# Performance work log

Measured on AMD Instinct MI355X. Metric: run time of the kernel, lower is better.

The kernel has to match this reference:

```python
import jax, jax.numpy as jnp
import numpy as np

GAMMA = 1.0

def setup_inputs() -> dict:
    key = jax.random.key(0)
    kx, ky = jax.random.split(key)
    x = jax.random.normal(kx, (8192, 64), dtype=jnp.float32)
    y = jax.random.normal(ky, (8192, 64), dtype=jnp.float32)
    return {"x": x, "y": y}

def reference(x, y):
    # RBF kernel K[b,a] = exp(-gamma * ||x_b - y_a||^2)
    # broadcast intermediate of the naive formulation (same math).
    x_sq = jnp.sum(x * x, axis=-1)                    # (B,)
    y_sq = jnp.sum(y * y, axis=-1)                    # (A,)
    xy = jnp.einsum('bd,ad->ba', x, y)                # (B, A) GEMM
    dist_sq = x_sq[:, None] + y_sq[None, :] - 2.0 * xy
    dist_sq = jnp.maximum(dist_sq, 0.0)               # numeric floor
    return jnp.exp(-GAMMA * dist_sq)
```

## Files before the change

### kernel.cpp

```cpp
#include <hip/hip_runtime.h>

#define D    64
#define BM   128
#define BN   128
#define NROW 8192

typedef _Float16 f16x8 __attribute__((ext_vector_type(8)));
typedef float    f32x4 __attribute__((ext_vector_type(4)));

__global__ __launch_bounds__(256) void rbf_rowsq(const float* __restrict__ x,
                                                 const float* __restrict__ y,
                                                 float* __restrict__ sq) {
    int tid = blockIdx.x * blockDim.x + threadIdx.x;
    const float* src = (tid < NROW) ? x : y;
    int row = tid & (NROW - 1);
    const float4* p = reinterpret_cast<const float4*>(src + row * D);
    float s = 0.f;
#pragma unroll
    for (int i = 0; i < D / 4; ++i) {
        float4 v = p[i];
        s = fmaf(v.x, v.x, s);
        s = fmaf(v.y, v.y, s);
        s = fmaf(v.z, v.z, s);
        s = fmaf(v.w, v.w, s);
    }
    sq[tid] = s;
}

__global__ __launch_bounds__(256, 2) void rbf_main(const float* __restrict__ x,
                                                   const float* __restrict__ y,
                                                   const float* __restrict__ sq,
                                                   float* __restrict__ out) {
    __shared__ __align__(16) char smem[65536];
    char* const XH = smem;
    char* const XL = smem + 16384;
    char* const YH = smem + 32768;
    char* const YL = smem + 49152;

    const int t    = threadIdx.x;
    const int row0 = blockIdx.y * BM;
    const int col0 = blockIdx.x * BN;

    {
        const int r    = t & 127;
        const int half = t >> 7;
        const int swz  = (r & 7) << 4;
        const int rowoff = r * 128;
        const float* xp = x + (size_t)(row0 + r) * D + half * 32;
        const float* yp = y + (size_t)(col0 + r) * D + half * 32;
#pragma unroll
        for (int it = 0; it < 4; ++it) {
            const int off = rowoff + ((half * 64 + it * 16) ^ swz);
            float4 a0 = *reinterpret_cast<const float4*>(xp + it * 8);
            float4 a1 = *reinterpret_cast<const float4*>(xp + it * 8 + 4);
            float4 b0 = *reinterpret_cast<const float4*>(yp + it * 8);
            float4 b1 = *reinterpret_cast<const float4*>(yp + it * 8 + 4);
            float xa[8] = {a0.x, a0.y, a0.z, a0.w, a1.x, a1.y, a1.z, a1.w};
            float yb[8] = {b0.x, b0.y, b0.z, b0.w, b1.x, b1.y, b1.z, b1.w};
            f16x8 xh, xl, yh, yl;
#pragma unroll
            for (int j = 0; j < 8; ++j) {
                _Float16 h = (_Float16)xa[j];
                xh[j] = h;
                xl[j] = (_Float16)(xa[j] - (float)h);
                _Float16 g = (_Float16)yb[j];
                yh[j] = g;
                yl[j] = (_Float16)(yb[j] - (float)g);
            }
            *reinterpret_cast<f16x8*>(XH + off) = xh;
            *reinterpret_cast<f16x8*>(XL + off) = xl;
            *reinterpret_cast<f16x8*>(YH + off) = yh;
            *reinterpret_cast<f16x8*>(YL + off) = yl;
        }
    }
    __syncthreads();

    const int lane = t & 63;
    const int w    = t >> 6;
    const int l15  = lane & 15;
    const int lg   = lane >> 4;
    const int swz  = (l15 & 7) << 4;

    const int arow0 = w * 32 + l15;
    const int arow1 = arow0 + 16;

    f32x4 acc[2][8];
#pragma unroll
    for (int i = 0; i < 2; ++i)
#pragma unroll
        for (int j = 0; j < 8; ++j) acc[i][j] = (f32x4){0.f, 0.f, 0.f, 0.f};

#pragma unroll
    for (int kh = 0; kh < 2; ++kh) {
        const int dsw = (kh * 64 + lg * 16) ^ swz;
        f16x8 ah0 = *reinterpret_cast<const f16x8*>(XH + arow0 * 128 + dsw);
        f16x8 ah1 = *reinterpret_cast<const f16x8*>(XH + arow1 * 128 + dsw);
        f16x8 al0 = *reinterpret_cast<const f16x8*>(XL + arow0 * 128 + dsw);
        f16x8 al1 = *reinterpret_cast<const f16x8*>(XL + arow1 * 128 + dsw);
#pragma unroll
        for (int nt = 0; nt < 8; ++nt) {
            const int boff = (nt * 16 + l15) * 128 + dsw;
            f16x8 bh = *reinterpret_cast<const f16x8*>(YH + boff);
            f16x8 bl = *reinterpret_cast<const f16x8*>(YL + boff);
            acc[0][nt] = __builtin_amdgcn_mfma_f32_16x16x32_f16(ah0, bh, acc[0][nt], 0, 0, 0);
            acc[1][nt] = __builtin_amdgcn_mfma_f32_16x16x32_f16(ah1, bh, acc[1][nt], 0, 0, 0);
            acc[0][nt] = __builtin_amdgcn_mfma_f32_16x16x32_f16(ah0, bl, acc[0][nt], 0, 0, 0);
            acc[1][nt] = __builtin_amdgcn_mfma_f32_16x16x32_f16(ah1, bl, acc[1][nt], 0, 0, 0);
            acc[0][nt] = __builtin_amdgcn_mfma_f32_16x16x32_f16(al0, bh, acc[0][nt], 0, 0, 0);
            acc[1][nt] = __builtin_amdgcn_mfma_f32_16x16x32_f16(al1, bh, acc[1][nt], 0, 0, 0);
        }
    }

    float xsqv[2][4], ysqv[8];
#pragma unroll
    for (int mt = 0; mt < 2; ++mt)
#pragma unroll
        for (int r = 0; r < 4; ++r)
            xsqv[mt][r] = sq[row0 + w * 32 + mt * 16 + lg * 4 + r];
#pragma unroll
    for (int nt = 0; nt < 8; ++nt)
        ysqv[nt] = sq[NROW + col0 + nt * 16 + l15];

#pragma unroll
    for (int mt = 0; mt < 2; ++mt) {
#pragma unroll
        for (int r = 0; r < 4; ++r) {
            const int rowg = row0 + w * 32 + mt * 16 + lg * 4 + r;
            float* op = out + (size_t)rowg * NROW + col0 + l15;
#pragma unroll
            for (int nt = 0; nt < 8; ++nt) {
                float d2 = fmaf(-2.f, acc[mt][nt][r], xsqv[mt][r] + ysqv[nt]);
                d2 = fmaxf(d2, 0.f);
                op[nt * 16] = __expf(-d2);
            }
        }
    }
}

extern "C" void kernel_launch(void* const* d_in, const int* in_sizes, int n_in,
                              void* d_out, int out_size, void* d_ws, size_t ws_size,
                              hipStream_t stream) {
    const float* x = (const float*)d_in[0];
    const float* y = (const float*)d_in[1];
    float* out = (float*)d_out;
    float* sq  = (float*)d_ws;

    rbf_rowsq<<<64, 256, 0, stream>>>(x, y, sq);
    rbf_main<<<dim3(NROW / BN, NROW / BM), 256, 0, stream>>>(x, y, sq, out);
}
```

Baseline: 72.69 us.

## Fuse row-norm kernel into main RBF kernel, keep X in registers, vectorize stores

Removes the separate row-squared-norm kernel and computes x and y norms inside the main kernel, with x norms reduced by lane shuffles and y norms kept in shared memory. X fragments are now loaded straight into registers, so shared memory drops to 32KB and occupancy can rise to 3 blocks per CU. The MFMA operands are swapped so each lane holds 4 consecutive output columns, which allows float4 output stores in place of scalar ones. The cost is redundant norm computation in every block and higher register pressure.

```diff
diff --git a/kernel.cpp b/kernel.cpp
--- a/kernel.cpp
+++ b/kernel.cpp
@@ -1,138 +1,121 @@
 #include <hip/hip_runtime.h>
 
 #define D    64
-#define BM   128
-#define BN   128
 #define NROW 8192
 
 typedef _Float16 f16x8 __attribute__((ext_vector_type(8)));
 typedef float    f32x4 __attribute__((ext_vector_type(4)));
 
-__global__ __launch_bounds__(256) void rbf_rowsq(const float* __restrict__ x,
-                                                 const float* __restrict__ y,
-                                                 float* __restrict__ sq) {
-    int tid = blockIdx.x * blockDim.x + threadIdx.x;
-    const float* src = (tid < NROW) ? x : y;
-    int row = tid & (NROW - 1);
-    const float4* p = reinterpret_cast<const float4*>(src + row * D);
-    float s = 0.f;
-#pragma unroll
-    for (int i = 0; i < D / 4; ++i) {
-        float4 v = p[i];
-        s = fmaf(v.x, v.x, s);
-        s = fmaf(v.y, v.y, s);
-        s = fmaf(v.z, v.z, s);
-        s = fmaf(v.w, v.w, s);
-    }
-    sq[tid] = s;
-}
-
-__global__ __launch_bounds__(256, 2) void rbf_main(const float* __restrict__ x,
-                                                   const float* __restrict__ y,
-                                                   const float* __restrict__ sq,
-                                                   float* __restrict__ out) {
-    __shared__ __align__(16) char smem[65536];
-    char* const XH = smem;
-    char* const XL = smem + 16384;
-    char* const YH = smem + 32768;
-    char* const YL = smem + 49152;
+__global__ __launch_bounds__(256, 3) void rbf_fused(const float* __restrict__ x,
+                                                    const float* __restrict__ y,
+                                                    float* __restrict__ out) {
+    __shared__ __align__(16) char YH[16384];
+    __shared__ __align__(16) char YL[16384];
+    __shared__ float Ysq0[128];
+    __shared__ float Ysq1[128];
 
     const int t    = threadIdx.x;
-    const int row0 = blockIdx.y * BM;
-    const int col0 = blockIdx.x * BN;
+    const int col0 = blockIdx.x * 128;
+    const int row0 = blockIdx.y * 128;
 
     {
         const int r    = t & 127;
         const int half = t >> 7;
         const int swz  = (r & 7) << 4;
-        const int rowoff = r * 128;
-        const float* xp = x + (size_t)(row0 + r) * D + half * 32;
         const float* yp = y + (size_t)(col0 + r) * D + half * 32;
+        float ssq = 0.f;
 #pragma unroll
         for (int it = 0; it < 4; ++it) {
-            const int off = rowoff + ((half * 64 + it * 16) ^ swz);
-            float4 a0 = *reinterpret_cast<const float4*>(xp + it * 8);
-            float4 a1 = *reinterpret_cast<const float4*>(xp + it * 8 + 4);
             float4 b0 = *reinterpret_cast<const float4*>(yp + it * 8);
             float4 b1 = *reinterpret_cast<const float4*>(yp + it * 8 + 4);
-            float xa[8] = {a0.x, a0.y, a0.z, a0.w, a1.x, a1.y, a1.z, a1.w};
-            float yb[8] = {b0.x, b0.y, b0.z, b0.w, b1.x, b1.y, b1.z, b1.w};
-            f16x8 xh, xl, yh, yl;
+            float v[8] = {b0.x, b0.y, b0.z, b0.w, b1.x, b1.y, b1.z, b1.w};
+            f16x8 h, l;
 #pragma unroll
             for (int j = 0; j < 8; ++j) {
-                _Float16 h = (_Float16)xa[j];
-                xh[j] = h;
-                xl[j] = (_Float16)(xa[j] - (float)h);
-                _Float16 g = (_Float16)yb[j];
-                yh[j] = g;
-                yl[j] = (_Float16)(yb[j] - (float)g);
+                _Float16 hh = (_Float16)v[j];
+                h[j] = hh;
+                l[j] = (_Float16)(v[j] - (float)hh);
+                ssq  = fmaf(v[j], v[j], ssq);
             }
-            *reinterpret_cast<f16x8*>(XH + off) = xh;
-            *reinterpret_cast<f16x8*>(XL + off) = xl;
-            *reinterpret_cast<f16x8*>(YH + off) = yh;
-            *reinterpret_cast<f16x8*>(YL + off) = yl;
+            const int off = r * 128 + ((half * 64 + it * 16) ^ swz);
+            *reinterpret_cast<f16x8*>(YH + off) = h;
+            *reinterpret_cast<f16x8*>(YL + off) = l;
         }
+        if (half == 0) Ysq0[r] = ssq; else Ysq1[r] = ssq;
     }
-    __syncthreads();
 
     const int lane = t & 63;
     const int w    = t >> 6;
     const int l15  = lane & 15;
     const int lg   = lane >> 4;
-    const int swz  = (l15 & 7) << 4;
 
-    const int arow0 = w * 32 + l15;
-    const int arow1 = arow0 + 16;
+    f16x8 xh[2][2], xl[2][2];
+    float xsq[2];
+#pragma unroll
+    for (int i = 0; i < 2; ++i) {
+        const float* xp = x + (size_t)(row0 + w * 32 + i * 16 + l15) * D + lg * 8;
+        float s = 0.f;
+#pragma unroll
+        for (int kh = 0; kh < 2; ++kh) {
+            float4 a0 = *reinterpret_cast<const float4*>(xp + kh * 32);
+            float4 a1 = *reinterpret_cast<const float4*>(xp + kh * 32 + 4);
+            float v[8] = {a0.x, a0.y, a0.z, a0.w, a1.x, a1.y, a1.z, a1.w};
+#pragma unroll
+            for (int j = 0; j < 8; ++j) {
+                _Float16 hh = (_Float16)v[j];
+                xh[i][kh][j] = hh;
+                xl[i][kh][j] = (_Float16)(v[j] - (float)hh);
+                s = fmaf(v[j], v[j], s);
+            }
+        }
+        s += __shfl_xor(s, 16);
+        s += __shfl_xor(s, 32);
+        xsq[i] = s;
+    }
+    __syncthreads();
 
     f32x4 acc[2][8];
 #pragma unroll
     for (int i = 0; i < 2; ++i)
 #pragma unroll
-        for (int j = 0; j < 8; ++j) acc[i][j] = (f32x4){0.f, 0.f, 0.f, 0.f};
+        for (int nt = 0; nt < 8; ++nt) acc[i][nt] = (f32x4){0.f, 0.f, 0.f, 0.f};
 
+    const int swzA = (l15 & 7) << 4;
 #pragma unroll
     for (int kh = 0; kh < 2; ++kh) {
-        const int dsw = (kh * 64 + lg * 16) ^ swz;
-        f16x8 ah0 = *reinterpret_cast<const f16x8*>(XH + arow0 * 128 + dsw);
-        f16x8 ah1 = *reinterpret_cast<const f16x8*>(XH + arow1 * 128 + dsw);
-        f16x8 al0 = *reinterpret_cast<const f16x8*>(XL + arow0 * 128 + dsw);
-        f16x8 al1 = *reinterpret_cast<const f16x8*>(XL + arow1 * 128 + dsw);
+        const int dsw = (kh * 64 + lg * 16) ^ swzA;
 #pragma unroll
         for (int nt = 0; nt < 8; ++nt) {
-            const int boff = (nt * 16 + l15) * 128 + dsw;
-            f16x8 bh = *reinterpret_cast<const f16x8*>(YH + boff);
-            f16x8 bl = *reinterpret_cast<const f16x8*>(YL + boff);
-            acc[0][nt] = __builtin_amdgcn_mfma_f32_16x16x32_f16(ah0, bh, acc[0][nt], 0, 0, 0);
-            acc[1][nt] = __builtin_amdgcn_mfma_f32_16x16x32_f16(ah1, bh, acc[1][nt], 0, 0, 0);
-            acc[0][nt] = __builtin_amdgcn_mfma_f32_16x16x32_f16(ah0, bl, acc[0][nt], 0, 0, 0);
-            acc[1][nt] = __builtin_amdgcn_mfma_f32_16x16x32_f16(ah1, bl, acc[1][nt], 0, 0, 0);
-            acc[0][nt] = __builtin_amdgcn_mfma_f32_16x16x32_f16(al0, bh, acc[0][nt], 0, 0, 0);
-            acc[1][nt] = __builtin_amdgcn_mfma_f32_16x16x32_f16(al1, bh, acc[1][nt], 0, 0, 0);
+            const int aoff = (nt * 16 + l15) * 128 + dsw;
+            f16x8 yh = *reinterpret_cast<const f16x8*>(YH + aoff);
+            f16x8 yl = *reinterpret_cast<const f16x8*>(YL + aoff);
+            acc[0][nt] = __builtin_amdgcn_mfma_f32_16x16x32_f16(yh, xh[0][kh], acc[0][nt], 0, 0, 0);
+            acc[1][nt] = __builtin_amdgcn_mfma_f32_16x16x32_f16(yh, xh[1][kh], acc[1][nt], 0, 0, 0);
+            acc[0][nt] = __builtin_amdgcn_mfma_f32_16x16x32_f16(yl, xh[0][kh], acc[0][nt], 0, 0, 0);
+            acc[1][nt] = __builtin_amdgcn_mfma_f32_16x16x32_f16(yl, xh[1][kh], acc[1][nt], 0, 0, 0);
+            acc[0][nt] = __builtin_amdgcn_mfma_f32_16x16x32_f16(yh, xl[0][kh], acc[0][nt], 0, 0, 0);
+            acc[1][nt] = __builtin_amdgcn_mfma_f32_16x16x32_f16(yh, xl[1][kh], acc[1][nt], 0, 0, 0);
         }
     }
 
-    float xsqv[2][4], ysqv[8];
 #pragma unroll
-    for (int mt = 0; mt < 2; ++mt)
+    for (int nt = 0; nt < 8; ++nt) {
+        const int c = nt * 16 + lg * 4;
+        float4 p0 = *reinterpret_cast<const float4*>(&Ysq0[c]);
+        float4 p1 = *reinterpret_cast<const float4*>(&Ysq1[c]);
+        float ysqv[4] = {p0.x + p1.x, p0.y + p1.y, p0.z + p1.z, p0.w + p1.w};
 #pragma unroll
-        for (int r = 0; r < 4; ++r)
-            xsqv[mt][r] = sq[row0 + w * 32 + mt * 16 + lg * 4 + r];
+        for (int i = 0; i < 2; ++i) {
+            const int rowg = row0 + w * 32 + i * 16 + l15;
+            float e[4];
 #pragma unroll
-    for (int nt = 0; nt < 8; ++nt)
-        ysqv[nt] = sq[NROW + col0 + nt * 16 + l15];
-
-#pragma unroll
-    for (int mt = 0; mt < 2; ++mt) {
-#pragma unroll
-        for (int r = 0; r < 4; ++r) {
-            const int rowg = row0 + w * 32 + mt * 16 + lg * 4 + r;
-            float* op = out + (size_t)rowg * NROW + col0 + l15;
-#pragma unroll
-            for (int nt = 0; nt < 8; ++nt) {
-                float d2 = fmaf(-2.f, acc[mt][nt][r], xsqv[mt][r] + ysqv[nt]);
+            for (int r = 0; r < 4; ++r) {
+                float d2 = fmaf(-2.f, acc[i][nt][r], xsq[i] + ysqv[r]);
                 d2 = fmaxf(d2, 0.f);
-                op[nt * 16] = __expf(-d2);
+                e[r] = __expf(-d2);
             }
+            *reinterpret_cast<float4*>(out + (size_t)rowg * NROW + col0 + c) =
+                make_float4(e[0], e[1], e[2], e[3]);
         }
     }
 }
@@ -143,8 +126,7 @@
     const float* x = (const float*)d_in[0];
     const float* y = (const float*)d_in[1];
     float* out = (float*)d_out;
-    float* sq  = (float*)d_ws;
+    (void)d_ws; (void)ws_size;
 
-    rbf_rowsq<<<64, 256, 0, stream>>>(x, y, sq);
-    rbf_main<<<dim3(NROW / BN, NROW / BM), 256, 0, stream>>>(x, y, sq, out);
+    rbf_fused<<<dim3(NROW / 128, NROW / 128), 256, 0, stream>>>(x, y, out);
 }
```

New measurement: 67.22 us. 1.08x faster.
